# Performance work log

Hardware: AMD Instinct MI355X
Metric: run time of the kernel (lower is better)

Reference implementation:

```python
import jax, jax.numpy as jnp
import numpy as np

N_SRC = 200000
N_DST = 50000
N_EDGES = 800000
N_IN = 256
N_OUT = 128


def setup_inputs() -> dict:
    key = jax.random.key(0)
    ks = jax.random.split(key, 10)
    x = jax.random.normal(ks[0], (N_SRC, N_IN), dtype=jnp.float32)
    edge_rows = jax.random.randint(ks[1], (N_EDGES,), 0, N_DST, dtype=jnp.int32)
    edge_cols = jax.random.randint(ks[2], (N_EDGES,), 0, N_SRC, dtype=jnp.int32)
    edge_vals = jax.random.uniform(ks[3], (N_EDGES,), dtype=jnp.float32)
    sampled_nodes = jax.random.randint(ks[4], (N_DST,), 0, N_SRC, dtype=jnp.int32)
    W_w = jax.random.normal(ks[5], (N_IN, N_OUT), dtype=jnp.float32) * 0.05
    b_w = jax.random.normal(ks[6], (N_OUT,), dtype=jnp.float32) * 0.05
    W_b = jax.random.normal(ks[7], (N_IN, N_OUT), dtype=jnp.float32) * 0.05
    b_b = jax.random.normal(ks[8], (N_OUT,), dtype=jnp.float32) * 0.05
    scale = jnp.ones((2 * N_OUT,), dtype=jnp.float32)
    offset = jnp.zeros((2 * N_OUT,), dtype=jnp.float32)
    return {"x": x, "edge_rows": edge_rows, "edge_cols": edge_cols,
            "edge_vals": edge_vals, "sampled_nodes": sampled_nodes,
            "W_w": W_w, "b_w": b_w, "W_b": W_b, "b_b": b_b,
            "scale": scale, "offset": offset}


def reference(x, edge_rows, edge_cols, edge_vals, sampled_nodes,
              W_w, b_w, W_b, b_b, scale, offset):
    # SpMM: feat[r] = sum_e vals[e] * x[cols[e]] for rows[e]==r  -> [N_DST, N_IN]
    msgs = edge_vals[:, None] * x[edge_cols]
    feat = jax.ops.segment_sum(msgs, edge_rows, num_segments=N_DST)
    # dual linear + concat -> [N_DST, 2*N_OUT]
    self_part = x[sampled_nodes] @ W_b + b_b
    neigh_part = feat @ W_w + b_w
    out = jax.nn.elu(jnp.concatenate([self_part, neigh_part], axis=1))
    # row-wise normalize (biased variance), then affine
    mean = out.mean(axis=1, keepdims=True)
    var = out.var(axis=1, keepdims=True) + 1e-9
    return (out - mean) * scale * jax.lax.rsqrt(var) + offset
```

## Files before the change

kernel.cpp:

```cpp
#include <hip/hip_runtime.h>
#include <math.h>

#define N_SRC   200000
#define N_DST   50000
#define N_EDGES 800000
#define N_IN    256
#define N_OUT   128
#define CAP     64

#define WS_CNT   0
#define WS_WTW   204800
#define WS_WTB   270336
#define WS_SELF  335872
#define WS_Y     13135872
#define WS_CSR   64335872

typedef short  bf16x8 __attribute__((ext_vector_type(8)));
typedef unsigned short u16x8 __attribute__((ext_vector_type(8)));
typedef float  f32x4  __attribute__((ext_vector_type(4)));

__device__ inline unsigned short f2bf(float f) {
    unsigned u = __builtin_bit_cast(unsigned, f);
    u += 0x7fffu + ((u >> 16) & 1u);
    return (unsigned short)(u >> 16);
}
__device__ inline float bf2f(unsigned short h) {
    return __builtin_bit_cast(float, (unsigned)h << 16);
}

__global__ __launch_bounds__(256) void k_init(const float* __restrict__ Ww,
                                              const float* __restrict__ Wb,
                                              unsigned short* __restrict__ Wtw,
                                              unsigned short* __restrict__ Wtb,
                                              int* __restrict__ cnt) {
    int tot = blockIdx.x * 256 + threadIdx.x;
    int sel = tot >> 15;
    int idx = tot & 32767;
    int n = idx >> 8, k = idx & 255;
    const float* src = sel ? Wb : Ww;
    unsigned short* dst = sel ? Wtb : Wtw;
    dst[n * 256 + k] = f2bf(src[k * 128 + n]);
    if (tot < N_DST) cnt[tot] = 0;
}

#define GSCAT 3125
#define GBIG  3125
#define GSELF 782
#define EPS 132

__global__ __launch_bounds__(256, 4) void k_mega(
        const float* __restrict__ x,
        const int* __restrict__ erows, const int* __restrict__ ecols,
        const float* __restrict__ evals, const int* __restrict__ sn,
        const unsigned short* __restrict__ Wtw, const unsigned short* __restrict__ Wtb,
        int* __restrict__ cnt, int2* __restrict__ csr_pad,
        unsigned short* __restrict__ ybuf, unsigned short* __restrict__ selfp) {
    __shared__ __align__(16) unsigned short sm[64 * EPS];
    const int tid = threadIdx.x;

    if (blockIdx.x < GSCAT) {
        int i = blockIdx.x * 256 + tid;
        int r = erows[i];
        int rank = atomicAdd(&cnt[r], 1);
        if (rank < CAP) {
            int2 cv;
            cv.x = ecols[i];
            cv.y = __builtin_bit_cast(int, evals[i]);
            csr_pad[r * CAP + rank] = cv;
        }
        return;
    }

    const int gb = blockIdx.x - GSCAT;
    const bool isBig = gb < GBIG;
    const int* rowidx = isBig ? nullptr : sn;
    const unsigned short* Bt = isBig ? Wtw : Wtb;
    unsigned short* Y = isBig ? ybuf : selfp;
    const int M = isBig ? N_SRC : N_DST;
    const int bid = isBig ? gb : gb - GBIG;

    const int lane = tid & 63, wid = tid >> 6;
    const int l15 = lane & 15, quad = lane >> 4;
    const int row0 = bid * 64;

    int srow = row0 + wid * 16 + l15;
    if (srow >= M) srow = M - 1;
    if (rowidx) srow = rowidx[srow];
    const float*          ap = x  + (long)srow * 256 + quad * 8;
    const unsigned short* bp = Bt + (long)l15 * 256 + quad * 8;

    f32x4 acc[8];
    #pragma unroll
    for (int t = 0; t < 8; t++) acc[t] = (f32x4){0.f, 0.f, 0.f, 0.f};

    #pragma unroll
    for (int kt = 0; kt < 8; kt++) {
        const int k0 = kt * 32;
        float4 a0 = *(const float4*)(ap + k0);
        float4 a1 = *(const float4*)(ap + k0 + 4);
        bf16x8 bfr[8];
        #pragma unroll
        for (int t = 0; t < 8; t++)
            bfr[t] = *(const bf16x8*)(bp + (long)t * 4096 + k0);
        bf16x8 af;
        af[0] = (short)f2bf(a0.x); af[1] = (short)f2bf(a0.y);
        af[2] = (short)f2bf(a0.z); af[3] = (short)f2bf(a0.w);
        af[4] = (short)f2bf(a1.x); af[5] = (short)f2bf(a1.y);
        af[6] = (short)f2bf(a1.z); af[7] = (short)f2bf(a1.w);
        #pragma unroll
        for (int t = 0; t < 8; t++)
            acc[t] = __builtin_amdgcn_mfma_f32_16x16x32_bf16(af, bfr[t], acc[t], 0, 0, 0);
    }

    #pragma unroll
    for (int t = 0; t < 8; t++)
        #pragma unroll
        for (int rg = 0; rg < 4; rg++)
            sm[(wid * 16 + quad * 4 + rg) * EPS + t * 16 + l15] = f2bf(acc[t][rg]);
    __syncthreads();
    const int orow = tid >> 2, oc0 = (tid & 3) * 32;
    if (row0 + orow < M) {
        unsigned short* dst = Y + (long)(row0 + orow) * 128 + oc0;
        #pragma unroll
        for (int i = 0; i < 4; i++)
            *(u16x8*)(dst + i * 8) = *(const u16x8*)&sm[orow * EPS + oc0 + i * 8];
    }
}

#define GATHER(j) \
    int   c##j = __shfl(cv.x, e0 + j, 64); \
    float v##j = __builtin_bit_cast(float, __shfl(cv.y, e0 + j, 64)); \
    unsigned p##j = *(const unsigned*)(y + (long)c##j * 128 + (lane << 1));
#define ACCUM(j) \
    a0 = fmaf(v##j, __builtin_bit_cast(float, p##j << 16), a0); \
    a1 = fmaf(v##j, __builtin_bit_cast(float, p##j & 0xffff0000u), a1);

__global__ __launch_bounds__(256) void k_sage(const unsigned short* __restrict__ y,
                                              const unsigned short* __restrict__ selfp,
                                              const int* __restrict__ cnt,
                                              const int2* __restrict__ csr_pad,
                                              const float* __restrict__ bw,
                                              const float* __restrict__ bb,
                                              const float* __restrict__ scale,
                                              const float* __restrict__ offs,
                                              float* __restrict__ out) {
    const int tid = threadIdx.x, lane = tid & 63, wid = tid >> 6;
    const int row = blockIdx.x * 4 + wid;
    const int m = min(cnt[row], CAP);

    int2 cv = (lane < m) ? csr_pad[(long)row * CAP + lane] : make_int2(0, 0);

    unsigned spk = *(const unsigned*)(selfp + (long)row * 128 + lane * 2);
    float s0 = bf2f((unsigned short)(spk & 0xffff)) + bb[lane * 2];
    float s1 = bf2f((unsigned short)(spk >> 16))    + bb[lane * 2 + 1];
    s0 = s0 > 0.f ? s0 : expm1f(s0);
    s1 = s1 > 0.f ? s1 : expm1f(s1);

    float a0 = 0.f, a1 = 0.f;
    const int mm = (m + 7) & ~7;
    for (int e0 = 0; e0 < mm; e0 += 8) {
        GATHER(0) GATHER(1) GATHER(2) GATHER(3)
        GATHER(4) GATHER(5) GATHER(6) GATHER(7)
        ACCUM(0) ACCUM(1) ACCUM(2) ACCUM(3)
        ACCUM(4) ACCUM(5) ACCUM(6) ACCUM(7)
    }
    a0 += bw[lane * 2];
    a1 += bw[lane * 2 + 1];
    a0 = a0 > 0.f ? a0 : expm1f(a0);
    a1 = a1 > 0.f ? a1 : expm1f(a1);

    float s  = s0 + s1 + a0 + a1;
    float s2 = s0 * s0 + s1 * s1 + a0 * a0 + a1 * a1;
    #pragma unroll
    for (int o = 32; o > 0; o >>= 1) {
        s  += __shfl_xor(s,  o, 64);
        s2 += __shfl_xor(s2, o, 64);
    }
    float mean = s * (1.f / 256.f);
    float var  = s2 * (1.f / 256.f) - mean * mean;
    float rstd = rsqrtf(var + 1e-9f);

    float* orow = out + (long)row * 256;
    float2 w0, w1;
    w0.x = (s0 - mean) * rstd * scale[lane * 2]           + offs[lane * 2];
    w0.y = (s1 - mean) * rstd * scale[lane * 2 + 1]       + offs[lane * 2 + 1];
    w1.x = (a0 - mean) * rstd * scale[128 + lane * 2]     + offs[128 + lane * 2];
    w1.y = (a1 - mean) * rstd * scale[128 + lane * 2 + 1] + offs[128 + lane * 2 + 1];
    *(float2*)(orow + lane * 2)       = w0;
    *(float2*)(orow + 128 + lane * 2) = w1;
}

extern "C" void kernel_launch(void* const* d_in, const int* in_sizes, int n_in,
                              void* d_out, int out_size, void* d_ws, size_t ws_size,
                              hipStream_t stream) {
    const float* x     = (const float*)d_in[0];
    const int*   erows = (const int*)  d_in[1];
    const int*   ecols = (const int*)  d_in[2];
    const float* evals = (const float*)d_in[3];
    const int*   sn    = (const int*)  d_in[4];
    const float* Ww    = (const float*)d_in[5];
    const float* bw    = (const float*)d_in[6];
    const float* Wb    = (const float*)d_in[7];
    const float* bb    = (const float*)d_in[8];
    const float* scale = (const float*)d_in[9];
    const float* offs  = (const float*)d_in[10];
    float* out = (float*)d_out;

    char* ws = (char*)d_ws;
    int*   cnt     = (int*)  (ws + WS_CNT);
    unsigned short* Wtw   = (unsigned short*)(ws + WS_WTW);
    unsigned short* Wtb   = (unsigned short*)(ws + WS_WTB);
    unsigned short* selfp = (unsigned short*)(ws + WS_SELF);
    unsigned short* ybuf  = (unsigned short*)(ws + WS_Y);
    int2*  csr_pad = (int2*) (ws + WS_CSR);

    k_init <<<256, 256, 0, stream>>>(Ww, Wb, Wtw, Wtb, cnt);
    k_mega <<<GSCAT + GBIG + GSELF, 256, 0, stream>>>(x, erows, ecols, evals, sn,
                                                      Wtw, Wtb, cnt, csr_pad, ybuf, selfp);
    k_sage <<<N_DST / 4, 256, 0, stream>>>(ybuf, selfp, cnt, csr_pad,
                                           bw, bb, scale, offs, out);
}
```

Measured before the change: 489.1 us.

## Stage transposed weight tile in swizzled LDS and prefetch all A rows

The GEMM part of the fused kernel now copies the full 128x256 bf16 weight matrix into a 64KB XOR-swizzled LDS buffer, with two-phase loads. MFMA B fragments are then read from LDS instead of global memory. All 16 float4 activation loads per lane are issued up front to raise memory-level parallelism. Launch bounds drop to 2 blocks per CU because of the larger LDS footprint, which lowers occupancy. Each block also has to reload the full weight matrix (64KB) per 64-row tile.

```diff
diff --git a/kernel.cpp b/kernel.cpp
--- a/kernel.cpp
+++ b/kernel.cpp
@@ -48,14 +48,16 @@
 #define GSELF 782
 #define EPS 132
 
-__global__ __launch_bounds__(256, 4) void k_mega(
+#define BSWZ(row, chunk) ((row) * 256 + (((chunk) ^ ((row) & 7)) << 3))
+
+__global__ __launch_bounds__(256, 2) void k_mega(
         const float* __restrict__ x,
         const int* __restrict__ erows, const int* __restrict__ ecols,
         const float* __restrict__ evals, const int* __restrict__ sn,
         const unsigned short* __restrict__ Wtw, const unsigned short* __restrict__ Wtb,
         int* __restrict__ cnt, int2* __restrict__ csr_pad,
         unsigned short* __restrict__ ybuf, unsigned short* __restrict__ selfp) {
-    __shared__ __align__(16) unsigned short sm[64 * EPS];
+    __shared__ __align__(16) unsigned short sm[32768];
     const int tid = threadIdx.x;
 
     if (blockIdx.x < GSCAT) {
@@ -86,32 +88,58 @@
     int srow = row0 + wid * 16 + l15;
     if (srow >= M) srow = M - 1;
     if (rowidx) srow = rowidx[srow];
-    const float*          ap = x  + (long)srow * 256 + quad * 8;
-    const unsigned short* bp = Bt + (long)l15 * 256 + quad * 8;
+    const float* ap = x + (long)srow * 256 + quad * 8;
 
     f32x4 acc[8];
     #pragma unroll
     for (int t = 0; t < 8; t++) acc[t] = (f32x4){0.f, 0.f, 0.f, 0.f};
 
+    u16x8 bst[8];
+    #pragma unroll
+    for (int j = 0; j < 8; j++)
+        bst[j] = ((const u16x8*)Bt)[j * 256 + tid];
+    float4 areg[16];
     #pragma unroll
     for (int kt = 0; kt < 8; kt++) {
-        const int k0 = kt * 32;
-        float4 a0 = *(const float4*)(ap + k0);
-        float4 a1 = *(const float4*)(ap + k0 + 4);
-        bf16x8 bfr[8];
-        #pragma unroll
-        for (int t = 0; t < 8; t++)
-            bfr[t] = *(const bf16x8*)(bp + (long)t * 4096 + k0);
+        areg[2 * kt]     = *(const float4*)(ap + kt * 32);
+        areg[2 * kt + 1] = *(const float4*)(ap + kt * 32 + 4);
+    }
+    __builtin_amdgcn_sched_barrier(0);
+
+    #pragma unroll
+    for (int j = 0; j < 8; j++) {
+        int slot = j * 256 + tid;
+        *(u16x8*)&sm[BSWZ(slot >> 5, slot & 31)] = bst[j];
+    }
+    #pragma unroll
+    for (int j = 0; j < 8; j++)
+        bst[j] = ((const u16x8*)Bt)[(j + 8) * 256 + tid];
+    __builtin_amdgcn_sched_barrier(0);
+    #pragma unroll
+    for (int j = 0; j < 8; j++) {
+        int slot = (j + 8) * 256 + tid;
+        *(u16x8*)&sm[BSWZ(slot >> 5, slot & 31)] = bst[j];
+    }
+    __syncthreads();
+
+    #pragma unroll
+    for (int kt = 0; kt < 8; kt++) {
+        float4 a0 = areg[2 * kt], a1 = areg[2 * kt + 1];
         bf16x8 af;
         af[0] = (short)f2bf(a0.x); af[1] = (short)f2bf(a0.y);
         af[2] = (short)f2bf(a0.z); af[3] = (short)f2bf(a0.w);
         af[4] = (short)f2bf(a1.x); af[5] = (short)f2bf(a1.y);
         af[6] = (short)f2bf(a1.z); af[7] = (short)f2bf(a1.w);
+        const int chunk = kt * 4 + quad;
         #pragma unroll
-        for (int t = 0; t < 8; t++)
-            acc[t] = __builtin_amdgcn_mfma_f32_16x16x32_bf16(af, bfr[t], acc[t], 0, 0, 0);
-    }
-
+        for (int t = 0; t < 8; t++) {
+            const int row = t * 16 + l15;
+            bf16x8 bfv = *(const bf16x8*)&sm[BSWZ(row, chunk)];
+            acc[t] = __builtin_amdgcn_mfma_f32_16x16x32_bf16(af, bfv, acc[t], 0, 0, 0);
+        }
+    }
+
+    __syncthreads();
     #pragma unroll
     for (int t = 0; t < 8; t++)
         #pragma unroll
```

After: 414.4 us. -15.3%, faster.
